# Optimization experiments

Measured on AMD Instinct MI355X. Metric: run time of the kernel, lower is better.

## Reference

```python
import jax, jax.numpy as jnp
import numpy as np

LOG2 = np.float32(np.log(2.0))

def _jsd_pos(p):
    # get_positive_expectation, measure='JSD', average=False
    return LOG2 - jax.nn.softplus(-p)

def setup_inputs() -> dict:
    key = jax.random.key(0)
    k1, k2, k3, k4, k5, k6 = jax.random.split(key, 6)
    N, G, D = 65536, 512, 256
    batch_1 = jnp.sort(jax.random.randint(k1, (N,), 0, G))
    batch_2 = jnp.sort(jax.random.randint(k2, (N,), 0, G))
    z1 = jax.random.normal(k3, (N, D), dtype=jnp.float32)
    z2 = jax.random.normal(k4, (N, D), dtype=jnp.float32)
    g1 = jax.random.normal(k5, (G, D), dtype=jnp.float32)
    g2 = jax.random.normal(k6, (G, D), dtype=jnp.float32)
    return {"batch_1": batch_1, "batch_2": batch_2, "z1": z1, "z2": z2, "g1": g1, "g2": g2}

def reference(batch_1, batch_2, z1, z2, g1, g2):
    # pos_mask scatter-build -> dense one-hot [N, G]
    pos_mask_1 = jax.nn.one_hot(batch_1, g1.shape[0], dtype=z1.dtype)
    pos_mask_2 = jax.nn.one_hot(batch_2, g2.shape[0], dtype=z2.dtype)
    # masked node-graph similarity matrices [N, G]
    self_sim_1 = (z1 @ g1.T) * pos_mask_1
    self_sim_2 = (z2 @ g2.T) * pos_mask_2
    cross_sim_12 = (z1 @ g2.T) * pos_mask_1
    cross_sim_21 = (z2 @ g1.T) * pos_mask_2
    # sep=True branch: per-node row sums, L2 distance over nodes
    self_js_11 = _jsd_pos(self_sim_1).sum(1)
    cross_js_12 = _jsd_pos(cross_sim_12).sum(1)
    self_js_22 = _jsd_pos(self_sim_2).sum(1)
    cross_js_21 = _jsd_pos(cross_sim_21).sum(1)
    L_1 = jnp.sqrt(jnp.sum((self_js_11 - cross_js_12) ** 2))
    L_2 = jnp.sqrt(jnp.sum((self_js_22 - cross_js_21) ** 2))
    return L_1 + L_2
```

## Files before the change

### kernel.cpp

```cpp
#include <hip/hip_runtime.h>
#include <math.h>

__device__ __forceinline__ float spn(float p) {
    return fmaxf(-p, 0.0f) + __logf(1.0f + __expf(-fabsf(p)));
}

__device__ __forceinline__ float dot4(float4 a, float4 b) {
    return a.x * b.x + a.y * b.y + a.z * b.z + a.w * b.w;
}

__device__ __forceinline__ float wave64_reduce(float x) {
    int t;
    t = __builtin_amdgcn_update_dpp(0, __builtin_bit_cast(int, x), 0x111, 0xf, 0xf, true);
    x += __builtin_bit_cast(float, t);
    t = __builtin_amdgcn_update_dpp(0, __builtin_bit_cast(int, x), 0x112, 0xf, 0xf, true);
    x += __builtin_bit_cast(float, t);
    t = __builtin_amdgcn_update_dpp(0, __builtin_bit_cast(int, x), 0x114, 0xf, 0xf, true);
    x += __builtin_bit_cast(float, t);
    t = __builtin_amdgcn_update_dpp(0, __builtin_bit_cast(int, x), 0x118, 0xf, 0xf, true);
    x += __builtin_bit_cast(float, t);
    t = __builtin_amdgcn_update_dpp(0, __builtin_bit_cast(int, x), 0x142, 0xa, 0xf, true);
    x += __builtin_bit_cast(float, t);
    t = __builtin_amdgcn_update_dpp(0, __builtin_bit_cast(int, x), 0x143, 0xc, 0xf, true);
    x += __builtin_bit_cast(float, t);
    return x;
}

#define NBLOCKS 4096
#define NODES_PER_WAVE 4

__global__ __launch_bounds__(256) void jsd_dot_kernel(
    const int*   __restrict__ b1,
    const int*   __restrict__ b2,
    const float* __restrict__ z1,
    const float* __restrict__ z2,
    const float* __restrict__ g1,
    const float* __restrict__ g2,
    float*       __restrict__ partials)
{
    const int wave = threadIdx.x >> 6;
    const int lane = threadIdx.x & 63;
    const int w    = blockIdx.x * 4 + wave;
    const int base = w * NODES_PER_WAVE;

    const int sbase = __builtin_amdgcn_readfirstlane(base);

    int i1[NODES_PER_WAVE], i2[NODES_PER_WAVE];
    #pragma unroll
    for (int j = 0; j < NODES_PER_WAVE; ++j) {
        i1[j] = b1[sbase + j];
        i2[j] = b2[sbase + j];
    }

    float4 a1[NODES_PER_WAVE], a2[NODES_PER_WAVE];
    #pragma unroll
    for (int j = 0; j < NODES_PER_WAVE; ++j) {
        a1[j] = ((const float4*)(z1 + (size_t)(sbase + j) * 256))[lane];
        a2[j] = ((const float4*)(z2 + (size_t)(sbase + j) * 256))[lane];
    }

    float acc1 = 0.0f, acc2 = 0.0f;

    #pragma unroll
    for (int j = 0; j < NODES_PER_WAVE; ++j) {
        const float4 w11 = ((const float4*)(g1 + (size_t)i1[j] * 256))[lane];
        const float4 w12 = ((const float4*)(g2 + (size_t)i1[j] * 256))[lane];
        const float4 w22 = ((const float4*)(g2 + (size_t)i2[j] * 256))[lane];
        const float4 w21 = ((const float4*)(g1 + (size_t)i2[j] * 256))[lane];

        float s11 = wave64_reduce(dot4(a1[j], w11));
        float c12 = wave64_reduce(dot4(a1[j], w12));
        float s22 = wave64_reduce(dot4(a2[j], w22));
        float c21 = wave64_reduce(dot4(a2[j], w21));

        if (lane == 63) {
            float d1 = spn(c12) - spn(s11);
            float d2 = spn(c21) - spn(s22);
            acc1 += d1 * d1;
            acc2 += d2 * d2;
        }
    }

    __shared__ float s1[4], s2[4];
    if (lane == 63) { s1[wave] = acc1; s2[wave] = acc2; }
    __syncthreads();

    if (threadIdx.x == 0) {
        partials[blockIdx.x * 2 + 0] = s1[0] + s1[1] + s1[2] + s1[3];
        partials[blockIdx.x * 2 + 1] = s2[0] + s2[1] + s2[2] + s2[3];
    }
}

__global__ __launch_bounds__(256) void jsd_reduce_kernel(
    const float* __restrict__ partials,
    float*       __restrict__ out)
{
    const int tid  = threadIdx.x;
    const int wave = tid >> 6;
    const int lane = tid & 63;

    float a = 0.0f, b = 0.0f;
    #pragma unroll
    for (int i = 0; i < NBLOCKS / 256; ++i) {
        a += partials[(i * 256 + tid) * 2 + 0];
        b += partials[(i * 256 + tid) * 2 + 1];
    }

    a = wave64_reduce(a);
    b = wave64_reduce(b);

    __shared__ float s1[4], s2[4];
    if (lane == 63) { s1[wave] = a; s2[wave] = b; }
    __syncthreads();

    if (tid == 0) {
        float t1 = s1[0] + s1[1] + s1[2] + s1[3];
        float t2 = s2[0] + s2[1] + s2[2] + s2[3];
        out[0] = sqrtf(t1) + sqrtf(t2);
    }
}

extern "C" void kernel_launch(void* const* d_in, const int* in_sizes, int n_in,
                              void* d_out, int out_size, void* d_ws, size_t ws_size,
                              hipStream_t stream) {
    const int*   b1 = (const int*)  d_in[0];
    const int*   b2 = (const int*)  d_in[1];
    const float* z1 = (const float*)d_in[2];
    const float* z2 = (const float*)d_in[3];
    const float* g1 = (const float*)d_in[4];
    const float* g2 = (const float*)d_in[5];
    float* out      = (float*)d_out;
    float* partials = (float*)d_ws;

    jsd_dot_kernel<<<NBLOCKS, 256, 0, stream>>>(b1, b2, z1, z2, g1, g2, partials);
    jsd_reduce_kernel<<<1, 256, 0, stream>>>(partials, out);
}
```

Measured before the change: 153.0 us.

## Process 16 nodes per wave with run-based graph-row reuse and z prefetch

Each wave now handles 16 consecutive nodes instead of 4, with 1024 blocks instead of 4096. Because batch indices are sorted, the wave keeps the last-loaded g1/g2 rows in registers and reloads them only when the graph index changes. The next node's z rows are loaded one iteration ahead so their latency overlaps with the current reductions. This cuts redundant gather traffic and per-block overhead, at the cost of fewer waves in flight to hide memory latency and more serialized work per wave.

```diff
diff --git a/kernel.cpp b/kernel.cpp
--- a/kernel.cpp
+++ b/kernel.cpp
@@ -1,5 +1,10 @@
 #include <hip/hip_runtime.h>
 #include <math.h>
+
+#define D 256
+#define NBLOCKS 1024
+#define WAVES 4
+#define NPW 16
 
 __device__ __forceinline__ float spn(float p) {
     return fmaxf(-p, 0.0f) + __logf(1.0f + __expf(-fabsf(p)));
@@ -26,10 +31,7 @@
     return x;
 }
 
-#define NBLOCKS 4096
-#define NODES_PER_WAVE 4
-
-__global__ __launch_bounds__(256) void jsd_dot_kernel(
+__global__ __launch_bounds__(256) void jsd_dot_run_kernel(
     const int*   __restrict__ b1,
     const int*   __restrict__ b2,
     const float* __restrict__ z1,
@@ -40,38 +42,54 @@
 {
     const int wave = threadIdx.x >> 6;
     const int lane = threadIdx.x & 63;
-    const int w    = blockIdx.x * 4 + wave;
-    const int base = w * NODES_PER_WAVE;
+    const int w    = blockIdx.x * WAVES + wave;
 
-    const int sbase = __builtin_amdgcn_readfirstlane(base);
+    const int sbase = __builtin_amdgcn_readfirstlane(w * NPW);
 
-    int i1[NODES_PER_WAVE], i2[NODES_PER_WAVE];
+    int i1v[NPW], i2v[NPW];
     #pragma unroll
-    for (int j = 0; j < NODES_PER_WAVE; ++j) {
-        i1[j] = b1[sbase + j];
-        i2[j] = b2[sbase + j];
+    for (int j = 0; j < NPW; ++j) {
+        i1v[j] = b1[sbase + j];
+        i2v[j] = b2[sbase + j];
     }
 
-    float4 a1[NODES_PER_WAVE], a2[NODES_PER_WAVE];
-    #pragma unroll
-    for (int j = 0; j < NODES_PER_WAVE; ++j) {
-        a1[j] = ((const float4*)(z1 + (size_t)(sbase + j) * 256))[lane];
-        a2[j] = ((const float4*)(z2 + (size_t)(sbase + j) * 256))[lane];
-    }
+    const float4* z1p = (const float4*)(z1 + (size_t)sbase * D);
+    const float4* z2p = (const float4*)(z2 + (size_t)sbase * D);
 
     float acc1 = 0.0f, acc2 = 0.0f;
 
+    int ci1 = -1, ci2 = -1;
+    float4 w11, w12, w22, w21;
+
+    float4 a1n = z1p[lane];
+    float4 a2n = z2p[lane];
+
     #pragma unroll
-    for (int j = 0; j < NODES_PER_WAVE; ++j) {
-        const float4 w11 = ((const float4*)(g1 + (size_t)i1[j] * 256))[lane];
-        const float4 w12 = ((const float4*)(g2 + (size_t)i1[j] * 256))[lane];
-        const float4 w22 = ((const float4*)(g2 + (size_t)i2[j] * 256))[lane];
-        const float4 w21 = ((const float4*)(g1 + (size_t)i2[j] * 256))[lane];
+    for (int j = 0; j < NPW; ++j) {
+        const float4 a1 = a1n;
+        const float4 a2 = a2n;
+        if (j + 1 < NPW) {
+            a1n = z1p[(j + 1) * (D / 4) + lane];
+            a2n = z2p[(j + 1) * (D / 4) + lane];
+        }
 
-        float s11 = wave64_reduce(dot4(a1[j], w11));
-        float c12 = wave64_reduce(dot4(a1[j], w12));
-        float s22 = wave64_reduce(dot4(a2[j], w22));
-        float c21 = wave64_reduce(dot4(a2[j], w21));
+        const int i1 = i1v[j];
+        const int i2 = i2v[j];
+        if (i1 != ci1) {
+            w11 = ((const float4*)(g1 + (size_t)i1 * D))[lane];
+            w12 = ((const float4*)(g2 + (size_t)i1 * D))[lane];
+            ci1 = i1;
+        }
+        if (i2 != ci2) {
+            w22 = ((const float4*)(g2 + (size_t)i2 * D))[lane];
+            w21 = ((const float4*)(g1 + (size_t)i2 * D))[lane];
+            ci2 = i2;
+        }
+
+        float s11 = wave64_reduce(dot4(a1, w11));
+        float c12 = wave64_reduce(dot4(a1, w12));
+        float s22 = wave64_reduce(dot4(a2, w22));
+        float c21 = wave64_reduce(dot4(a2, w21));
 
         if (lane == 63) {
             float d1 = spn(c12) - spn(s11);
@@ -81,13 +99,16 @@
         }
     }
 
-    __shared__ float s1[4], s2[4];
+    __shared__ float s1[WAVES], s2[WAVES];
     if (lane == 63) { s1[wave] = acc1; s2[wave] = acc2; }
     __syncthreads();
 
     if (threadIdx.x == 0) {
-        partials[blockIdx.x * 2 + 0] = s1[0] + s1[1] + s1[2] + s1[3];
-        partials[blockIdx.x * 2 + 1] = s2[0] + s2[1] + s2[2] + s2[3];
+        float t1 = 0.0f, t2 = 0.0f;
+        #pragma unroll
+        for (int k = 0; k < WAVES; ++k) { t1 += s1[k]; t2 += s2[k]; }
+        partials[blockIdx.x * 2 + 0] = t1;
+        partials[blockIdx.x * 2 + 1] = t2;
     }
 }
 
@@ -132,6 +153,6 @@
     float* out      = (float*)d_out;
     float* partials = (float*)d_ws;
 
-    jsd_dot_kernel<<<NBLOCKS, 256, 0, stream>>>(b1, b2, z1, z2, g1, g2, partials);
+    jsd_dot_run_kernel<<<NBLOCKS, 256, 0, stream>>>(b1, b2, z1, z2, g1, g2, partials);
     jsd_reduce_kernel<<<1, 256, 0, stream>>>(partials, out);
 }
```

Result: slower. 159.3 us (+4.2%).
